# Performance work log

Measured on AMD Instinct MI355X. Metric: run time of the kernel, lower is better.

Reference implementation:

```python
import jax, jax.numpy as jnp
import numpy as np

T = 4096
C = 2048
N_FEAT = 2048
NEG = -1e30  # finite stand-in for -inf so fully-masked (padding) rows stay NaN-free


def setup_inputs() -> dict:
    key = jax.random.key(0)
    kx, kw, kb = jax.random.split(key, 3)
    x = jax.random.normal(kx, (T, C), dtype=jnp.float32)
    # Dense(features=3*n_feat): kernel (C, 3*n_feat), bias (3*n_feat,)
    W = jax.random.normal(kw, (C, 3 * N_FEAT), dtype=jnp.float32) * (1.0 / np.sqrt(C))
    b = jax.random.normal(kb, (3 * N_FEAT,), dtype=jnp.float32) * 0.01
    n_padd = 128
    return {"x": x, "W": W, "b": b, "n_padd": n_padd}


def reference(x, W, b, n_padd):
    T_, _ = x.shape
    qkv = x @ W + b                      # (T, 3*n_feat)
    q, k, v = jnp.split(qkv, 3, axis=1)  # each (T, n_feat)
    scale = 1.0 / jnp.sqrt(jnp.float32(q.shape[1]))
    att = (q @ k.T) * scale              # (T, T)
    rows = jnp.arange(T_)[:, None]
    cols = jnp.arange(T_)[None, :]
    # causal AND both row/col past the left padding
    mask = (cols <= rows) & (cols >= n_padd) & (rows >= n_padd)
    att = jnp.where(mask, att, NEG)
    p = jax.nn.softmax(att, axis=1)      # stable row softmax
    # kernel only stores rows >= n_padd; padding rows are zero
    p = jnp.where(rows >= n_padd, p, 0.0)
    y = p @ v                            # (T, n_feat)
    return y
```

## Files before the change

kernel.cpp:

```cpp
#include <hip/hip_runtime.h>
#include <cstdint>


#define T_DIM 4096
#define C_DIM 2048
#define NF    2048
#define N3    6144
#define NEGV  (-1e30f)

typedef __bf16 bf16x8 __attribute__((ext_vector_type(8)));
typedef __bf16 bf16x4 __attribute__((ext_vector_type(4)));
typedef float  f32x4  __attribute__((ext_vector_type(4)));

__device__ __forceinline__ void async_cp16(const void* g, void* l) {
    __builtin_amdgcn_global_load_lds(
        reinterpret_cast<const __attribute__((address_space(1))) unsigned int*>(
            reinterpret_cast<uintptr_t>(g)),
        reinterpret_cast<__attribute__((address_space(3))) unsigned int*>(
            reinterpret_cast<uintptr_t>(l)),
        16, 0, 0);
}

__device__ __forceinline__ void gemm_loop(const __bf16* A, const __bf16* B,
                                          int lda, int ldb, int m0, int n0,
                                          int kiters, __bf16* As, __bf16* Bs,
                                          f32x4 (&acc)[4][4]) {
    const int t    = threadIdx.x;
    const int wv   = t >> 6;
    const int lane = t & 63;
    const int srow = t >> 3;
    const int scol = (((t & 7) ^ (srow & 7)) << 3);
    const int wm   = (wv >> 1) << 6;
    const int wn   = (wv & 1) << 6;
    const int lrow = lane & 15;
    const int kq   = lane >> 4;
    const int swz  = lrow & 7;
    const int rc0  = ((kq ^ swz) << 3);
    const int rc1  = (((kq | 4) ^ swz) << 3);

    const __bf16* ga = A + (size_t)(m0 + srow) * lda + scol;
    const __bf16* gb = B + (size_t)(n0 + srow) * ldb + scol;

    for (int kk = 0; kk < kiters; ++kk) {
#pragma unroll
        for (int i = 0; i < 4; ++i) {
            async_cp16(ga + (size_t)(32 * i) * lda, &As[i * 2048 + wv * 512]);
            async_cp16(gb + (size_t)(32 * i) * ldb, &Bs[i * 2048 + wv * 512]);
        }
        ga += 64; gb += 64;
        __syncthreads();

#pragma unroll
        for (int kb = 0; kb < 2; ++kb) {
            const int rc = kb ? rc1 : rc0;
            bf16x8 af[4], bfr[4];
#pragma unroll
            for (int mi = 0; mi < 4; ++mi)
                af[mi] = *(const bf16x8*)&As[(wm + mi * 16 + lrow) * 64 + rc];
#pragma unroll
            for (int ni = 0; ni < 4; ++ni)
                bfr[ni] = *(const bf16x8*)&Bs[(wn + ni * 16 + lrow) * 64 + rc];
#pragma unroll
            for (int mi = 0; mi < 4; ++mi)
#pragma unroll
                for (int ni = 0; ni < 4; ++ni)
                    acc[mi][ni] = __builtin_amdgcn_mfma_f32_16x16x32_bf16(
                        af[mi], bfr[ni], acc[mi][ni], 0, 0, 0);
        }
        __syncthreads();
    }
}

__global__ void prep_kernel(const float* __restrict__ x,
                            __bf16* __restrict__ xb,
                            const float* __restrict__ W,
                            __bf16* __restrict__ Wt) {
    if (blockIdx.x < 2048) {
        const int n4 = (T_DIM * C_DIM) / 4;
        const int stride = 2048 * 256;
        for (int i = blockIdx.x * 256 + threadIdx.x; i < n4; i += stride) {
            float4 v = ((const float4*)x)[i];
            bf16x4 o;
            o[0] = (__bf16)v.x; o[1] = (__bf16)v.y;
            o[2] = (__bf16)v.z; o[3] = (__bf16)v.w;
            ((bf16x4*)xb)[i] = o;
        }
        return;
    }
    __shared__ float tile[32][33];
    const int tb = blockIdx.x - 2048;
    const int bx = (tb % (N3 / 32)) * 32;
    const int by = (tb / (N3 / 32)) * 32;
    const int tx = threadIdx.x & 31, ty = threadIdx.x >> 5;
#pragma unroll
    for (int i = 0; i < 32; i += 8)
        tile[ty + i][tx] = W[(size_t)(by + ty + i) * N3 + bx + tx];
    __syncthreads();
#pragma unroll
    for (int i = 0; i < 32; i += 8)
        Wt[(size_t)(bx + ty + i) * C_DIM + by + tx] = (__bf16)tile[tx][ty + i];
}

#define EPILOG_SETUP()                                     \
    const int t = threadIdx.x, wv = t >> 6, lane = t & 63; \
    const int wm = (wv >> 1) << 6, wn = (wv & 1) << 6;     \
    const int rq = (lane >> 4) << 2, cn = lane & 15

__global__ void __launch_bounds__(256)
qkv_gemm_kernel(const __bf16* __restrict__ xb, const __bf16* __restrict__ Wt,
                const float* __restrict__ bias, __bf16* __restrict__ qb,
                __bf16* __restrict__ kb, __bf16* __restrict__ vT) {
    __shared__ __bf16 As[128 * 64];
    __shared__ __bf16 Bs[128 * 64];
    f32x4 acc[4][4] = {};
    const int m0 = blockIdx.x * 128, n0 = blockIdx.y * 128;
    gemm_loop(xb, Wt, C_DIM, C_DIM, m0, n0, C_DIM / 64, As, Bs, acc);

    EPILOG_SETUP();
#pragma unroll
    for (int mi = 0; mi < 4; ++mi)
#pragma unroll
        for (int ni = 0; ni < 4; ++ni) {
            int col = n0 + wn + ni * 16 + cn;
            float bv = bias[col];
            if (col >= 2 * NF) {
                bf16x4 o;
#pragma unroll
                for (int r = 0; r < 4; ++r) o[r] = (__bf16)(acc[mi][ni][r] + bv);
                int row = m0 + wm + mi * 16 + rq;
                *(bf16x4*)&vT[(size_t)(col - 2 * NF) * T_DIM + row] = o;
            } else {
#pragma unroll
                for (int r = 0; r < 4; ++r) {
                    int row = m0 + wm + mi * 16 + rq + r;
                    float val = acc[mi][ni][r] + bv;
                    if (col < NF)
                        qb[(size_t)row * NF + col] = (__bf16)val;
                    else
                        kb[(size_t)row * NF + (col - NF)] = (__bf16)val;
                }
            }
        }
}

__global__ void __launch_bounds__(256)
sc_gemm_kernel(const __bf16* __restrict__ qb, const __bf16* __restrict__ kb,
               __bf16* __restrict__ S, const int* __restrict__ npadd_p) {
    int i = blockIdx.x;
    int mt = (int)((sqrtf(8.0f * (float)i + 1.0f) - 1.0f) * 0.5f);
    while ((mt + 1) * (mt + 2) / 2 <= i) ++mt;
    while (mt * (mt + 1) / 2 > i) --mt;
    int nt = i - mt * (mt + 1) / 2;
    const int m0 = mt * 128, n0 = nt * 128;
    const int npadd = *npadd_p;
    if (m0 + 128 <= npadd || n0 + 128 <= npadd) return;

    __shared__ __bf16 As[128 * 64];
    __shared__ __bf16 Bs[128 * 64];
    f32x4 acc[4][4] = {};
    gemm_loop(qb, kb, NF, NF, m0, n0, NF / 64, As, Bs, acc);

    const float scale = 0.022097086912079608f;
    EPILOG_SETUP();
#pragma unroll
    for (int mi = 0; mi < 4; ++mi)
#pragma unroll
        for (int ni = 0; ni < 4; ++ni) {
            int j = n0 + wn + ni * 16 + cn;
#pragma unroll
            for (int r = 0; r < 4; ++r) {
                int row = m0 + wm + mi * 16 + rq + r;
                S[(size_t)row * T_DIM + j] = (__bf16)(acc[mi][ni][r] * scale);
            }
        }
}

__global__ void __launch_bounds__(256)
softmax_kernel(const __bf16* __restrict__ S, __bf16* __restrict__ P,
               const int* __restrict__ npadd_p) {
    const int wv = threadIdx.x >> 6, lane = threadIdx.x & 63;
    const int row = blockIdx.x * 4 + wv;
    const int npadd = *npadd_p;
    __bf16* prow = P + (size_t)row * T_DIM;

    if (row < npadd) {
        bf16x8 z = {};
#pragma unroll
        for (int c = 0; c < 8; ++c) ((bf16x8*)prow)[c * 64 + lane] = z;
        return;
    }

    const __bf16* srow = S + (size_t)row * T_DIM;
    float vals[64];
    float mx = NEGV;
#pragma unroll
    for (int c = 0; c < 8; ++c) {
        if (c * 512 > row) {
#pragma unroll
            for (int e = 0; e < 8; ++e) vals[c * 8 + e] = NEGV;
            continue;
        }
        int j0 = c * 512 + lane * 8;
        bf16x8 v = ((const bf16x8*)srow)[c * 64 + lane];
#pragma unroll
        for (int e = 0; e < 8; ++e) {
            float f = (j0 + e >= npadd && j0 + e <= row) ? (float)v[e] : NEGV;
            vals[c * 8 + e] = f;
            mx = fmaxf(mx, f);
        }
    }
#pragma unroll
    for (int o = 32; o > 0; o >>= 1) mx = fmaxf(mx, __shfl_xor(mx, o));

    float sm = 0.f;
#pragma unroll
    for (int k = 0; k < 64; ++k) {
        vals[k] = exp2f((vals[k] - mx) * 1.4426950408889634f);
        sm += vals[k];
    }
#pragma unroll
    for (int o = 32; o > 0; o >>= 1) sm += __shfl_xor(sm, o);
    float inv = 1.0f / sm;

#pragma unroll
    for (int c = 0; c < 8; ++c) {
        bf16x8 o;
#pragma unroll
        for (int e = 0; e < 8; ++e) o[e] = (__bf16)(vals[c * 8 + e] * inv);
        ((bf16x8*)prow)[c * 64 + lane] = o;
    }
}

__global__ void __launch_bounds__(256)
pv_gemm_kernel(const __bf16* __restrict__ P, const __bf16* __restrict__ vT,
               float* __restrict__ out, const int* __restrict__ npadd_p) {
    const int idx = blockIdx.x;
    const int kskip = *npadd_p >> 6;
    int mt, nt, start, iters;
    bool atomic_out;
    if (idx < 256) {
        mt = idx & 15; nt = idx >> 4;
        int kt = (mt + 1) * 2 - kskip; if (kt < 0) kt = 0;
        start = kskip; iters = kt; atomic_out = false;
    } else {
        int j = idx - 256;
        mt = 16 + (j & 15); nt = (j >> 4) & 15;
        int half = j >> 8;
        int kt = (mt + 1) * 2 - kskip; if (kt < 0) kt = 0;
        int h0 = (kt + 1) >> 1;
        start = kskip + (half ? h0 : 0);
        iters = half ? kt - h0 : h0;
        atomic_out = true;
    }
    const int m0 = mt * 128, n0 = nt * 128;

    __shared__ __bf16 As[128 * 64];
    __shared__ __bf16 Bs[128 * 64];
    f32x4 acc[4][4] = {};
    gemm_loop(P + (size_t)start * 64, vT + (size_t)start * 64,
              T_DIM, T_DIM, m0, n0, iters, As, Bs, acc);

    EPILOG_SETUP();
#pragma unroll
    for (int mi = 0; mi < 4; ++mi)
#pragma unroll
        for (int ni = 0; ni < 4; ++ni) {
            int col = n0 + wn + ni * 16 + cn;
#pragma unroll
            for (int r = 0; r < 4; ++r) {
                int row = m0 + wm + mi * 16 + rq + r;
                float* p = &out[(size_t)row * NF + col];
                if (atomic_out) unsafeAtomicAdd(p, acc[mi][ni][r]);
                else            *p = acc[mi][ni][r];
            }
        }
}

extern "C" void kernel_launch(void* const* d_in, const int* in_sizes, int n_in,
                              void* d_out, int out_size, void* d_ws,
                              size_t ws_size, hipStream_t stream) {
    const float* x = (const float*)d_in[0];
    const float* W = (const float*)d_in[1];
    const float* b = (const float*)d_in[2];
    const int* npadd = (const int*)d_in[3];
    float* out = (float*)d_out;

    char* ws = (char*)d_ws;
    __bf16* xb = (__bf16*)(ws);
    __bf16* Wt = (__bf16*)(ws + (16ull << 20));
    __bf16* qb = (__bf16*)(ws + (40ull << 20));
    __bf16* kb = (__bf16*)(ws + (56ull << 20));
    __bf16* vT = (__bf16*)(ws + (72ull << 20));
    __bf16* S  = (__bf16*)(ws + (88ull << 20));
    __bf16* P  = (__bf16*)(ws + (40ull << 20));

    hipMemsetAsync(out + (size_t)2048 * NF, 0, (size_t)2048 * NF * 4, stream);

    prep_kernel<<<2048 + (N3 / 32) * (C_DIM / 32), 256, 0, stream>>>(x, xb, W, Wt);
    qkv_gemm_kernel<<<dim3(T_DIM / 128, N3 / 128), 256, 0, stream>>>(xb, Wt, b,
                                                                     qb, kb, vT);
    sc_gemm_kernel<<<528, 256, 0, stream>>>(qb, kb, S, npadd);
    softmax_kernel<<<T_DIM / 4, 256, 0, stream>>>(S, P, npadd);
    pv_gemm_kernel<<<768, 256, 0, stream>>>(P, vT, out, npadd);
}
```

Measured before the change: 348.4 us.

## Rewrite QKV GEMM with 256x128 tiles, 512 threads and triple-buffered async loads

The QKV projection GEMM now uses its own main loop with 256x128 output tiles per 512-thread block and a three-stage LDS ring filled by async global-to-LDS copies. A vmcnt wait plus one barrier per k-step overlaps the next loads with the MFMA work, and MFMA issue priority is raised during compute. The epilogue branch for V versus Q/K is now taken once per block instead of per element. This is meant to improve data reuse and hide memory latency, at the cost of a larger LDS footprint (~144KB) that may restrict occupancy.

```diff
diff --git a/kernel.cpp b/kernel.cpp
--- a/kernel.cpp
+++ b/kernel.cpp
@@ -106,33 +106,119 @@
     const int wm = (wv >> 1) << 6, wn = (wv & 1) << 6;     \
     const int rq = (lane >> 4) << 2, cn = lane & 15
 
-__global__ void __launch_bounds__(256)
+__global__ void __launch_bounds__(512)
 qkv_gemm_kernel(const __bf16* __restrict__ xb, const __bf16* __restrict__ Wt,
                 const float* __restrict__ bias, __bf16* __restrict__ qb,
                 __bf16* __restrict__ kb, __bf16* __restrict__ vT) {
-    __shared__ __bf16 As[128 * 64];
-    __shared__ __bf16 Bs[128 * 64];
+    __shared__ __bf16 As[3][256 * 64];
+    __shared__ __bf16 Bs[3][128 * 64];
+
+    const int t    = threadIdx.x;
+    const int wv   = t >> 6;
+    const int lane = t & 63;
+    const int srow = t >> 3;
+    const int scol = (((t & 7) ^ (srow & 7)) << 3);
+    const int m0   = blockIdx.x * 256;
+    const int n0   = blockIdx.y * 128;
+    const int wmo  = (wv >> 1) << 6;
+    const int wno  = (wv & 1) << 6;
+    const int lrow = lane & 15;
+    const int kq   = lane >> 4;
+    const int swz  = lrow & 7;
+    const int rc0  = ((kq ^ swz) << 3);
+    const int rc1  = (((kq | 4) ^ swz) << 3);
+
+    const __bf16* ga = xb + (size_t)(m0 + srow) * C_DIM + scol;
+    const __bf16* gb = Wt + (size_t)(n0 + srow) * C_DIM + scol;
+
     f32x4 acc[4][4] = {};
-    const int m0 = blockIdx.x * 128, n0 = blockIdx.y * 128;
-    gemm_loop(xb, Wt, C_DIM, C_DIM, m0, n0, C_DIM / 64, As, Bs, acc);
-
-    EPILOG_SETUP();
-#pragma unroll
-    for (int mi = 0; mi < 4; ++mi)
+
+    auto stage = [&](int kt, int s) {
+        const __bf16* a  = ga + kt * 64;
+        const __bf16* b2 = gb + kt * 64;
+#pragma unroll
+        for (int i = 0; i < 4; ++i)
+            async_cp16(a + (size_t)(64 * i) * C_DIM, &As[s][i * 4096 + wv * 512]);
+#pragma unroll
+        for (int i = 0; i < 2; ++i)
+            async_cp16(b2 + (size_t)(64 * i) * C_DIM, &Bs[s][i * 4096 + wv * 512]);
+    };
+
+    auto compute = [&](int s) {
+        const __bf16* Ab = As[s];
+        const __bf16* Bb = Bs[s];
+        bf16x8 af[4][2], bfr[4][2];
+#pragma unroll
+        for (int mi = 0; mi < 4; ++mi) {
+            const __bf16* r = &Ab[(wmo + mi * 16 + lrow) * 64];
+            af[mi][0] = *(const bf16x8*)&r[rc0];
+            af[mi][1] = *(const bf16x8*)&r[rc1];
+        }
 #pragma unroll
         for (int ni = 0; ni < 4; ++ni) {
-            int col = n0 + wn + ni * 16 + cn;
-            float bv = bias[col];
-            if (col >= 2 * NF) {
+            const __bf16* r = &Bb[(wno + ni * 16 + lrow) * 64];
+            bfr[ni][0] = *(const bf16x8*)&r[rc0];
+            bfr[ni][1] = *(const bf16x8*)&r[rc1];
+        }
+        __builtin_amdgcn_s_setprio(1);
+#pragma unroll
+        for (int kh = 0; kh < 2; ++kh)
+#pragma unroll
+            for (int mi = 0; mi < 4; ++mi)
+#pragma unroll
+                for (int ni = 0; ni < 4; ++ni)
+                    acc[mi][ni] = __builtin_amdgcn_mfma_f32_16x16x32_bf16(
+                        af[mi][kh], bfr[ni][kh], acc[mi][ni], 0, 0, 0);
+        __builtin_amdgcn_s_setprio(0);
+    };
+
+    constexpr int KT = C_DIM / 64;
+    stage(0, 0);
+    stage(1, 1);
+
+    int s0 = 0, s1 = 1, s2 = 2;
+    for (int kt = 0; kt < KT - 2; ++kt) {
+        asm volatile("s_waitcnt vmcnt(6)" ::: "memory");
+        __builtin_amdgcn_s_barrier();
+        asm volatile("" ::: "memory");
+        stage(kt + 2, s2);
+        compute(s0);
+        int tmp = s0; s0 = s1; s1 = s2; s2 = tmp;
+    }
+    asm volatile("s_waitcnt vmcnt(6)" ::: "memory");
+    __builtin_amdgcn_s_barrier();
+    asm volatile("" ::: "memory");
+    compute(s0);
+    { int tmp = s0; s0 = s1; s1 = s2; s2 = tmp; }
+    asm volatile("s_waitcnt vmcnt(0)" ::: "memory");
+    __builtin_amdgcn_s_barrier();
+    asm volatile("" ::: "memory");
+    compute(s0);
+
+    const int rq = (lane >> 4) << 2, cn = lane & 15;
+    if (n0 >= 2 * NF) {
+#pragma unroll
+        for (int mi = 0; mi < 4; ++mi)
+#pragma unroll
+            for (int ni = 0; ni < 4; ++ni) {
+                int col = n0 + wno + ni * 16 + cn;
+                float bv = bias[col];
                 bf16x4 o;
 #pragma unroll
                 for (int r = 0; r < 4; ++r) o[r] = (__bf16)(acc[mi][ni][r] + bv);
-                int row = m0 + wm + mi * 16 + rq;
+                int row = m0 + wmo + mi * 16 + rq;
                 *(bf16x4*)&vT[(size_t)(col - 2 * NF) * T_DIM + row] = o;
-            } else {
+            }
+    } else {
+#pragma unroll
+        for (int mi = 0; mi < 4; ++mi)
+#pragma unroll
+            for (int ni = 0; ni < 4; ++ni) {
+                int col = n0 + wno + ni * 16 + cn;
+                float bv = bias[col];
 #pragma unroll
                 for (int r = 0; r < 4; ++r) {
-                    int row = m0 + wm + mi * 16 + rq + r;
+                    int row = m0 + wmo + mi * 16 + rq + r;
                     float val = acc[mi][ni][r] + bv;
                     if (col < NF)
                         qb[(size_t)row * NF + col] = (__bf16)val;
@@ -140,7 +226,7 @@
                         kb[(size_t)row * NF + (col - NF)] = (__bf16)val;
                 }
             }
-        }
+    }
 }
 
 __global__ void __launch_bounds__(256)
@@ -297,7 +383,7 @@
     hipMemsetAsync(out + (size_t)2048 * NF, 0, (size_t)2048 * NF * 4, stream);
 
     prep_kernel<<<2048 + (N3 / 32) * (C_DIM / 32), 256, 0, stream>>>(x, xb, W, Wt);
-    qkv_gemm_kernel<<<dim3(T_DIM / 128, N3 / 128), 256, 0, stream>>>(xb, Wt, b,
+    qkv_gemm_kernel<<<dim3(T_DIM / 256, N3 / 128), 512, 0, stream>>>(xb, Wt, b,
                                                                      qb, kb, vT);
     sc_gemm_kernel<<<528, 256, 0, stream>>>(qb, kb, S, npadd);
     softmax_kernel<<<T_DIM / 4, 256, 0, stream>>>(S, P, npadd);
```

Result: faster. 335.4 us (-3.7%).

## Switch GEMMs to 256x256 tiles with double-buffered LDS and 8-wave ping-pong

Applied to the files above, without the earlier changes.

Replaces the 128x128 single-buffered GEMM loop with a 256x256 tile, 512-thread kernel that double-buffers A/B in LDS. The next K-slice is prefetched while the current one feeds MFMAs, with barriers and s_setprio interleaving loads and compute across waves. Work decomposition for the QKV, score and PV GEMMs is remapped to the larger tiles. This is meant to raise arithmetic intensity and hide global-load latency. In exchange the grids get much smaller (136 and 192 blocks), which can underfill the GPU's CUs, and the coarser causal tiles waste more masked work.

```diff
diff --git a/kernel.cpp b/kernel.cpp
--- a/kernel.cpp
+++ b/kernel.cpp
@@ -11,6 +11,9 @@
 typedef __bf16 bf16x8 __attribute__((ext_vector_type(8)));
 typedef __bf16 bf16x4 __attribute__((ext_vector_type(4)));
 typedef float  f32x4  __attribute__((ext_vector_type(4)));
+
+#define FENCE() asm volatile("" ::: "memory")
+#define BARRIER() do { FENCE(); __builtin_amdgcn_s_barrier(); FENCE(); } while (0)
 
 __device__ __forceinline__ void async_cp16(const void* g, void* l) {
     __builtin_amdgcn_global_load_lds(
@@ -21,17 +24,18 @@
         16, 0, 0);
 }
 
-__device__ __forceinline__ void gemm_loop(const __bf16* A, const __bf16* B,
-                                          int lda, int ldb, int m0, int n0,
-                                          int kiters, __bf16* As, __bf16* Bs,
-                                          f32x4 (&acc)[4][4]) {
+__device__ __forceinline__ void gemm256(const __bf16* A, const __bf16* B,
+                                        int lda, int ldb, int m0, int n0,
+                                        int kiters, __bf16* As, __bf16* Bs,
+                                        f32x4 (&acc)[8][4]) {
+    if (kiters <= 0) return;
     const int t    = threadIdx.x;
     const int wv   = t >> 6;
     const int lane = t & 63;
     const int srow = t >> 3;
     const int scol = (((t & 7) ^ (srow & 7)) << 3);
-    const int wm   = (wv >> 1) << 6;
-    const int wn   = (wv & 1) << 6;
+    const int wmo  = (wv >> 2) * 128;
+    const int wno  = (wv & 3) * 64;
     const int lrow = lane & 15;
     const int kq   = lane >> 4;
     const int swz  = lrow & 7;
@@ -41,35 +45,100 @@
     const __bf16* ga = A + (size_t)(m0 + srow) * lda + scol;
     const __bf16* gb = B + (size_t)(n0 + srow) * ldb + scol;
 
-    for (int kk = 0; kk < kiters; ++kk) {
-#pragma unroll
-        for (int i = 0; i < 4; ++i) {
-            async_cp16(ga + (size_t)(32 * i) * lda, &As[i * 2048 + wv * 512]);
-            async_cp16(gb + (size_t)(32 * i) * ldb, &Bs[i * 2048 + wv * 512]);
-        }
-        ga += 64; gb += 64;
-        __syncthreads();
-
-#pragma unroll
-        for (int kb = 0; kb < 2; ++kb) {
-            const int rc = kb ? rc1 : rc0;
-            bf16x8 af[4], bfr[4];
-#pragma unroll
-            for (int mi = 0; mi < 4; ++mi)
-                af[mi] = *(const bf16x8*)&As[(wm + mi * 16 + lrow) * 64 + rc];
+    auto stA4 = [&](int kk, int s) {
+        const __bf16* a = ga + kk * 64;
+#pragma unroll
+        for (int j = 0; j < 4; ++j)
+            async_cp16(a + (size_t)(64 * j) * lda,
+                       &As[s * 16384 + j * 4096 + wv * 512]);
+    };
+    auto stB4 = [&](int kk, int s) {
+        const __bf16* b2 = gb + kk * 64;
+#pragma unroll
+        for (int j = 0; j < 4; ++j)
+            async_cp16(b2 + (size_t)(64 * j) * ldb,
+                       &Bs[s * 16384 + j * 4096 + wv * 512]);
+    };
+    auto loadA4 = [&](const __bf16* Ab, int mh, int rc, bf16x8 (&af)[4]) {
+#pragma unroll
+        for (int mi = 0; mi < 4; ++mi)
+            af[mi] = *(const bf16x8*)
+                &Ab[(wmo + mh * 64 + mi * 16 + lrow) * 64 + rc];
+    };
+    auto loadB4 = [&](const __bf16* Bb, int rc, bf16x8 (&bfr)[4]) {
+#pragma unroll
+        for (int ni = 0; ni < 4; ++ni)
+            bfr[ni] = *(const bf16x8*)&Bb[(wno + ni * 16 + lrow) * 64 + rc];
+    };
+
+    bf16x8 af[4], bfr[4];
+
+    stA4(0, 0); stB4(0, 0);
+    asm volatile("s_waitcnt vmcnt(0)" ::: "memory");
+    BARRIER();
+
+    for (int kt = 0; kt < kiters; ++kt) {
+        const int b = kt & 1;
+        const __bf16* Ab = &As[b * 16384];
+        const __bf16* Bb = &Bs[b * 16384];
+        const bool pf = (kt + 1 < kiters);
+
+        loadB4(Bb, rc0, bfr);
+        loadA4(Ab, 0, rc0, af);
+        if (pf) stA4(kt + 1, b ^ 1);
+        BARRIER();
+        __builtin_amdgcn_s_setprio(1);
+#pragma unroll
+        for (int mi = 0; mi < 4; ++mi)
 #pragma unroll
             for (int ni = 0; ni < 4; ++ni)
-                bfr[ni] = *(const bf16x8*)&Bs[(wn + ni * 16 + lrow) * 64 + rc];
-#pragma unroll
-            for (int mi = 0; mi < 4; ++mi)
-#pragma unroll
-                for (int ni = 0; ni < 4; ++ni)
-                    acc[mi][ni] = __builtin_amdgcn_mfma_f32_16x16x32_bf16(
-                        af[mi], bfr[ni], acc[mi][ni], 0, 0, 0);
-        }
-        __syncthreads();
-    }
-}
+                acc[mi][ni] = __builtin_amdgcn_mfma_f32_16x16x32_bf16(
+                    af[mi], bfr[ni], acc[mi][ni], 0, 0, 0);
+        __builtin_amdgcn_s_setprio(0);
+        BARRIER();
+        loadA4(Ab, 1, rc0, af);
+        if (pf) stB4(kt + 1, b ^ 1);
+        BARRIER();
+        __builtin_amdgcn_s_setprio(1);
+#pragma unroll
+        for (int mi = 0; mi < 4; ++mi)
+#pragma unroll
+            for (int ni = 0; ni < 4; ++ni)
+                acc[4 + mi][ni] = __builtin_amdgcn_mfma_f32_16x16x32_bf16(
+                    af[mi], bfr[ni], acc[4 + mi][ni], 0, 0, 0);
+        __builtin_amdgcn_s_setprio(0);
+        BARRIER();
+        loadB4(Bb, rc1, bfr);
+        loadA4(Ab, 0, rc1, af);
+        BARRIER();
+        __builtin_amdgcn_s_setprio(1);
+#pragma unroll
+        for (int mi = 0; mi < 4; ++mi)
+#pragma unroll
+            for (int ni = 0; ni < 4; ++ni)
+                acc[mi][ni] = __builtin_amdgcn_mfma_f32_16x16x32_bf16(
+                    af[mi], bfr[ni], acc[mi][ni], 0, 0, 0);
+        __builtin_amdgcn_s_setprio(0);
+        BARRIER();
+        loadA4(Ab, 1, rc1, af);
+        BARRIER();
+        __builtin_amdgcn_s_setprio(1);
+#pragma unroll
+        for (int mi = 0; mi < 4; ++mi)
+#pragma unroll
+            for (int ni = 0; ni < 4; ++ni)
+                acc[4 + mi][ni] = __builtin_amdgcn_mfma_f32_16x16x32_bf16(
+                    af[mi], bfr[ni], acc[4 + mi][ni], 0, 0, 0);
+        __builtin_amdgcn_s_setprio(0);
+        if (pf) asm volatile("s_waitcnt vmcnt(0)" ::: "memory");
+        BARRIER();
+    }
+}
+
+#define EPI256()                                            \
+    const int t = threadIdx.x, wv = t >> 6, lane = t & 63;  \
+    const int wmo = (wv >> 2) * 128, wno = (wv & 3) * 64;   \
+    const int rq = (lane >> 4) << 2, cn = lane & 15
 
 __global__ void prep_kernel(const float* __restrict__ x,
                             __bf16* __restrict__ xb,
@@ -101,49 +170,52 @@
         Wt[(size_t)(bx + ty + i) * C_DIM + by + tx] = (__bf16)tile[tx][ty + i];
 }
 
-#define EPILOG_SETUP()                                     \
-    const int t = threadIdx.x, wv = t >> 6, lane = t & 63; \
-    const int wm = (wv >> 1) << 6, wn = (wv & 1) << 6;     \
-    const int rq = (lane >> 4) << 2, cn = lane & 15
-
-__global__ void __launch_bounds__(256)
+__global__ void __launch_bounds__(512)
 qkv_gemm_kernel(const __bf16* __restrict__ xb, const __bf16* __restrict__ Wt,
                 const float* __restrict__ bias, __bf16* __restrict__ qb,
                 __bf16* __restrict__ kb, __bf16* __restrict__ vT) {
-    __shared__ __bf16 As[128 * 64];
-    __shared__ __bf16 Bs[128 * 64];
-    f32x4 acc[4][4] = {};
-    const int m0 = blockIdx.x * 128, n0 = blockIdx.y * 128;
-    gemm_loop(xb, Wt, C_DIM, C_DIM, m0, n0, C_DIM / 64, As, Bs, acc);
-
-    EPILOG_SETUP();
-#pragma unroll
-    for (int mi = 0; mi < 4; ++mi)
-#pragma unroll
-        for (int ni = 0; ni < 4; ++ni) {
-            int col = n0 + wn + ni * 16 + cn;
-            float bv = bias[col];
-            if (col >= 2 * NF) {
+    __shared__ __bf16 As[2 * 256 * 64];
+    __shared__ __bf16 Bs[2 * 256 * 64];
+    f32x4 acc[8][4] = {};
+    const int m0 = blockIdx.x * 256;
+    const int by = blockIdx.y;
+    const int n0 = by * 256;
+    gemm256(xb, Wt, C_DIM, C_DIM, m0, n0, C_DIM / 64, As, Bs, acc);
+
+    EPI256();
+    if (by >= 16) {
+#pragma unroll
+        for (int mi = 0; mi < 8; ++mi)
+#pragma unroll
+            for (int ni = 0; ni < 4; ++ni) {
+                int col = n0 + wno + ni * 16 + cn;
+                float bv = bias[col];
                 bf16x4 o;
 #pragma unroll
                 for (int r = 0; r < 4; ++r) o[r] = (__bf16)(acc[mi][ni][r] + bv);
-                int row = m0 + wm + mi * 16 + rq;
+                int row = m0 + wmo + mi * 16 + rq;
                 *(bf16x4*)&vT[(size_t)(col - 2 * NF) * T_DIM + row] = o;
-            } else {
+            }
+    } else {
+        __bf16* dst = (by < 8) ? qb : kb;
+        const int coff = (by < 8) ? 0 : NF;
+#pragma unroll
+        for (int mi = 0; mi < 8; ++mi)
+#pragma unroll
+            for (int ni = 0; ni < 4; ++ni) {
+                int col = n0 + wno + ni * 16 + cn;
+                float bv = bias[col];
 #pragma unroll
                 for (int r = 0; r < 4; ++r) {
-                    int row = m0 + wm + mi * 16 + rq + r;
-                    float val = acc[mi][ni][r] + bv;
-                    if (col < NF)
-                        qb[(size_t)row * NF + col] = (__bf16)val;
-                    else
-                        kb[(size_t)row * NF + (col - NF)] = (__bf16)val;
+                    int row = m0 + wmo + mi * 16 + rq + r;
+                    dst[(size_t)row * NF + (col - coff)] =
+                        (__bf16)(acc[mi][ni][r] + bv);
                 }
             }
-        }
-}
-
-__global__ void __launch_bounds__(256)
+    }
+}
+
+__global__ void __launch_bounds__(512)
 sc_gemm_kernel(const __bf16* __restrict__ qb, const __bf16* __restrict__ kb,
                __bf16* __restrict__ S, const int* __restrict__ npadd_p) {
     int i = blockIdx.x;
@@ -151,25 +223,25 @@
     while ((mt + 1) * (mt + 2) / 2 <= i) ++mt;
     while (mt * (mt + 1) / 2 > i) --mt;
     int nt = i - mt * (mt + 1) / 2;
-    const int m0 = mt * 128, n0 = nt * 128;
+    const int m0 = mt * 256, n0 = nt * 256;
     const int npadd = *npadd_p;
-    if (m0 + 128 <= npadd || n0 + 128 <= npadd) return;
-
-    __shared__ __bf16 As[128 * 64];
-    __shared__ __bf16 Bs[128 * 64];
-    f32x4 acc[4][4] = {};
-    gemm_loop(qb, kb, NF, NF, m0, n0, NF / 64, As, Bs, acc);
+    if (m0 + 256 <= npadd || n0 + 256 <= npadd) return;
+
+    __shared__ __bf16 As[2 * 256 * 64];
+    __shared__ __bf16 Bs[2 * 256 * 64];
+    f32x4 acc[8][4] = {};
+    gemm256(qb, kb, NF, NF, m0, n0, NF / 64, As, Bs, acc);
 
     const float scale = 0.022097086912079608f;
-    EPILOG_SETUP();
-#pragma unroll
-    for (int mi = 0; mi < 4; ++mi)
+    EPI256();
+#pragma unroll
+    for (int mi = 0; mi < 8; ++mi)
 #pragma unroll
         for (int ni = 0; ni < 4; ++ni) {
-            int j = n0 + wn + ni * 16 + cn;
+            int j = n0 + wno + ni * 16 + cn;
 #pragma unroll
             for (int r = 0; r < 4; ++r) {
-                int row = m0 + wm + mi * 16 + rq + r;
+                int row = m0 + wmo + mi * 16 + rq + r;
                 S[(size_t)row * T_DIM + j] = (__bf16)(acc[mi][ni][r] * scale);
             }
         }
@@ -231,44 +303,44 @@
     }
 }
 
-__global__ void __launch_bounds__(256)
+__global__ void __launch_bounds__(512)
 pv_gemm_kernel(const __bf16* __restrict__ P, const __bf16* __restrict__ vT,
                float* __restrict__ out, const int* __restrict__ npadd_p) {
     const int idx = blockIdx.x;
     const int kskip = *npadd_p >> 6;
     int mt, nt, start, iters;
     bool atomic_out;
-    if (idx < 256) {
-        mt = idx & 15; nt = idx >> 4;
-        int kt = (mt + 1) * 2 - kskip; if (kt < 0) kt = 0;
-        start = kskip; iters = kt; atomic_out = false;
+    if (idx < 64) {
+        mt = idx >> 3; nt = idx & 7;
+        int ktt = (mt + 1) * 4 - kskip; if (ktt < 0) ktt = 0;
+        start = kskip; iters = ktt; atomic_out = false;
     } else {
-        int j = idx - 256;
-        mt = 16 + (j & 15); nt = (j >> 4) & 15;
-        int half = j >> 8;
-        int kt = (mt + 1) * 2 - kskip; if (kt < 0) kt = 0;
-        int h0 = (kt + 1) >> 1;
+        int j = idx - 64;
+        mt = 8 + ((j >> 3) & 7); nt = j & 7;
+        int half = j >> 6;
+        int ktt = (mt + 1) * 4 - kskip; if (ktt < 0) ktt = 0;
+        int h0 = (ktt + 1) >> 1;
         start = kskip + (half ? h0 : 0);
-        iters = half ? kt - h0 : h0;
+        iters = half ? ktt - h0 : h0;
         atomic_out = true;
     }
-    const int m0 = mt * 128, n0 = nt * 128;
-
-    __shared__ __bf16 As[128 * 64];
-    __shared__ __bf16 Bs[128 * 64];
-    f32x4 acc[4][4] = {};
-    gemm_loop(P + (size_t)start * 64, vT + (size_t)start * 64,
-              T_DIM, T_DIM, m0, n0, iters, As, Bs, acc);
-
-    EPILOG_SETUP();
-#pragma unroll
-    for (int mi = 0; mi < 4; ++mi)
+    const int m0 = mt * 256, n0 = nt * 256;
+
+    __shared__ __bf16 As[2 * 256 * 64];
+    __shared__ __bf16 Bs[2 * 256 * 64];
+    f32x4 acc[8][4] = {};
+    gemm256(P + (size_t)start * 64, vT + (size_t)start * 64,
+            T_DIM, T_DIM, m0, n0, iters, As, Bs, acc);
+
+    EPI256();
+#pragma unroll
+    for (int mi = 0; mi < 8; ++mi)
 #pragma unroll
         for (int ni = 0; ni < 4; ++ni) {
-            int col = n0 + wn + ni * 16 + cn;
+            int col = n0 + wno + ni * 16 + cn;
 #pragma unroll
             for (int r = 0; r < 4; ++r) {
-                int row = m0 + wm + mi * 16 + rq + r;
+                int row = m0 + wmo + mi * 16 + rq + r;
                 float* p = &out[(size_t)row * NF + col];
                 if (atomic_out) unsafeAtomicAdd(p, acc[mi][ni][r]);
                 else            *p = acc[mi][ni][r];
@@ -297,9 +369,9 @@
     hipMemsetAsync(out + (size_t)2048 * NF, 0, (size_t)2048 * NF * 4, stream);
 
     prep_kernel<<<2048 + (N3 / 32) * (C_DIM / 32), 256, 0, stream>>>(x, xb, W, Wt);
-    qkv_gemm_kernel<<<dim3(T_DIM / 128, N3 / 128), 256, 0, stream>>>(xb, Wt, b,
+    qkv_gemm_kernel<<<dim3(T_DIM / 256, N3 / 256), 512, 0, stream>>>(xb, Wt, b,
                                                                      qb, kb, vT);
-    sc_gemm_kernel<<<528, 256, 0, stream>>>(qb, kb, S, npadd);
+    sc_gemm_kernel<<<136, 512, 0, stream>>>(qb, kb, S, npadd);
     softmax_kernel<<<T_DIM / 4, 256, 0, stream>>>(S, P, npadd);
-    pv_gemm_kernel<<<768, 256, 0, stream>>>(P, vT, out, npadd);
-}
+    pv_gemm_kernel<<<192, 512, 0, stream>>>(P, vT, out, npadd);
+}
```

After: 379.8 us. 1.09x slower.
